# Performance work log

Measured on AMD Instinct MI355X. Metric: run time of the kernel, lower is better.

## Reference

```python
import jax, jax.numpy as jnp
import numpy as np

N_NODES = 50000
N_EDGES = 600000
IN_DIM, HID, OUT_DIM = 128, 128, 64


def setup_inputs() -> dict:
    key = jax.random.key(0)
    ks = jax.random.split(key, 12)
    h = jax.random.normal(ks[0], (N_NODES, IN_DIM), dtype=jnp.float32)
    src = jax.random.randint(ks[1], (N_EDGES,), 0, N_NODES, dtype=jnp.int32)
    dst = jax.random.randint(ks[2], (N_EDGES,), 0, N_NODES, dtype=jnp.int32)
    dims = [(IN_DIM, HID), (HID, HID), (HID, HID), (HID, OUT_DIM)]
    params = {}
    for i, (di, do) in enumerate(dims):
        scale = 1.0 / np.sqrt(di)
        params[f"W{i}"] = jax.random.uniform(ks[3 + i], (di, do), jnp.float32, -scale, scale)
        params[f"b{i}"] = jnp.zeros((do,), jnp.float32)
    return dict(h=h, src=src, dst=dst, **params)


def _gcn_layer(h, W, b, src, dst, norm_src, norm_dst, n_nodes):
    # DGL GraphConv, norm='both': D^{-1/2} A D^{-1/2} (h W) + b
    x = (h * norm_src) @ W              # [N, out]
    agg = jax.ops.segment_sum(x[src], dst, num_segments=n_nodes)
    return agg * norm_dst + b


def reference(h, src, dst, W0, b0, W1, b1, W2, b2, W3, b3):
    n = h.shape[0]
    ones = jnp.ones((src.shape[0],), h.dtype)
    deg_out = jnp.clip(jax.ops.segment_sum(ones, src, num_segments=n), 1.0)
    deg_in = jnp.clip(jax.ops.segment_sum(ones, dst, num_segments=n), 1.0)
    norm_src = (deg_out ** -0.5)[:, None]
    norm_dst = (deg_in ** -0.5)[:, None]
    Ws = [(W0, b0), (W1, b1), (W2, b2), (W3, b3)]
    for i, (W, b) in enumerate(Ws):
        h = _gcn_layer(h, W, b, src, dst, norm_src, norm_dst, n)
        if i != len(Ws) - 1:
            h = jax.nn.relu(h)  # dropout is identity in eval mode
    return h
```

## Files before the change

kernel.cpp:

```cpp
#include <hip/hip_runtime.h>


namespace {

constexpr int NN = 50000;
constexpr int NE = 600000;
constexpr int SCAN_BLK = 256;
constexpr int NBLK = (NN + SCAN_BLK - 1) / SCAN_BLK;
constexpr int EB = (NE + 255) / 256;
constexpr int MFMA0_BLOCKS = (NN / 16 + 3) / 4;
constexpr int WCVT_ELEMS = 16384 * 3 + 8192;
constexpr int WCVT_BLOCKS = WCVT_ELEMS / 256;

typedef unsigned short bhalf;
typedef __attribute__((ext_vector_type(8))) short short8v;
typedef __attribute__((ext_vector_type(4))) float f32x4;

__device__ inline float blo(unsigned int v) {
  return __uint_as_float(v << 16);
}
__device__ inline float bhi(unsigned int v) {
  return __uint_as_float(v & 0xFFFF0000u);
}
__device__ inline unsigned int f2b_bits(float f) {
  unsigned int b = __float_as_uint(f);
  return b + 0x7FFFu + ((b >> 16) & 1u);
}
__device__ inline unsigned int pack2(float lo, float hi) {
  return (f2b_bits(lo) >> 16) | (f2b_bits(hi) & 0xFFFF0000u);
}
__device__ inline bhalf f2b(float f) { return (bhalf)(f2b_bits(f) >> 16); }

__global__ __launch_bounds__(256) void wcvt_kernel(
    const float* __restrict__ W0, const float* __restrict__ W1,
    const float* __restrict__ W2, const float* __restrict__ W3,
    bhalf* __restrict__ wt0, bhalf* __restrict__ wt1,
    bhalf* __restrict__ wt2, bhalf* __restrict__ wt3) {
  int flat = blockIdx.x * 256 + threadIdx.x;
  if (flat < 16384) {
    int j = flat >> 7, k = flat & 127;
    wt0[flat] = f2b(W0[k * 128 + j]);
  } else if (flat < 32768) {
    int f = flat - 16384;
    int j = f >> 7, k = f & 127;
    wt1[f] = f2b(W1[k * 128 + j]);
  } else if (flat < 49152) {
    int f = flat - 32768;
    int j = f >> 7, k = f & 127;
    wt2[f] = f2b(W2[k * 128 + j]);
  } else {
    int f = flat - 49152;
    int j = f >> 7, k = f & 127;
    wt3[f] = f2b(W3[k * 64 + j]);
  }
}

__global__ __launch_bounds__(256, 4) void deg_gemm0_kernel(
    const int* __restrict__ src, const int* __restrict__ dst,
    int* __restrict__ dego, int* __restrict__ degi, int* __restrict__ le,
    const float* __restrict__ h, const bhalf* __restrict__ wt0,
    bhalf* __restrict__ x) {
  if (blockIdx.x < EB) {
    int e = blockIdx.x * 256 + threadIdx.x;
    if (e < NE) {
      atomicAdd(&dego[src[e]], 1);
      le[e] = atomicAdd(&degi[dst[e]], 1);
    }
    return;
  }
  const int lane = threadIdx.x & 63;
  const int wv = threadIdx.x >> 6;
  const int tile = (blockIdx.x - EB) * 4 + wv;
  if (tile >= NN / 16) return;
  const int row0 = tile * 16;
  const size_t arow = (size_t)(row0 + (lane & 15)) * 128;
  const int koff = (lane >> 4) * 8;
  const int bcol = lane & 15;

  f32x4 acc[8];
#pragma unroll
  for (int cf = 0; cf < 8; ++cf) acc[cf] = (f32x4){0.f, 0.f, 0.f, 0.f};

#pragma unroll
  for (int ks = 0; ks < 4; ++ks) {
    const int k0 = ks * 32 + koff;
    float4 ha = *reinterpret_cast<const float4*>(&h[arow + k0]);
    float4 hb = *reinterpret_cast<const float4*>(&h[arow + k0 + 4]);
    short8v av;
    av[0] = (short)f2b(ha.x); av[1] = (short)f2b(ha.y);
    av[2] = (short)f2b(ha.z); av[3] = (short)f2b(ha.w);
    av[4] = (short)f2b(hb.x); av[5] = (short)f2b(hb.y);
    av[6] = (short)f2b(hb.z); av[7] = (short)f2b(hb.w);
#pragma unroll
    for (int cf = 0; cf < 8; ++cf) {
      short8v bv = *reinterpret_cast<const short8v*>(
          &wt0[(size_t)(cf * 16 + bcol) * 128 + k0]);
      acc[cf] = __builtin_amdgcn_mfma_f32_16x16x32_bf16(av, bv, acc[cf], 0, 0, 0);
    }
  }

  const int crow = row0 + ((lane >> 4) << 2);
#pragma unroll
  for (int cf = 0; cf < 8; ++cf) {
#pragma unroll
    for (int r = 0; r < 4; ++r) {
      x[(size_t)(crow + r) * 128 + cf * 16 + bcol] = f2b(acc[cf][r]);
    }
  }
}

__global__ __launch_bounds__(SCAN_BLK) void scan1_norm(const int* __restrict__ dego,
                                                       const int* __restrict__ degi,
                                                       int* __restrict__ bsum,
                                                       float* __restrict__ ns,
                                                       float* __restrict__ nd) {
  __shared__ int ws[SCAN_BLK / 64];
  int i = blockIdx.x * SCAN_BLK + threadIdx.x;
  int v = 0;
  if (i < NN) {
    int din = degi[i];
    int dout = dego[i];
    v = din;
    int a = dout < 1 ? 1 : dout;
    int b = din < 1 ? 1 : din;
    ns[i] = 1.0f / sqrtf((float)a);
    nd[i] = 1.0f / sqrtf((float)b);
  }
#pragma unroll
  for (int off = 32; off; off >>= 1) v += __shfl_down(v, off, 64);
  int lane = threadIdx.x & 63, w = threadIdx.x >> 6;
  if (lane == 0) ws[w] = v;
  __syncthreads();
  if (threadIdx.x == 0) {
    int s = 0;
#pragma unroll
    for (int k = 0; k < SCAN_BLK / 64; ++k) s += ws[k];
    bsum[blockIdx.x] = s;
  }
}

__global__ __launch_bounds__(SCAN_BLK) void scan23(const int* __restrict__ deg,
                                                   const int* __restrict__ bsum,
                                                   int* __restrict__ rowptr) {
  __shared__ int sb[SCAN_BLK];
  __shared__ int s[SCAN_BLK];
  const int t = threadIdx.x;
  int vb = (t < NBLK) ? bsum[t] : 0;
  sb[t] = vb;
  __syncthreads();
  for (int off = 1; off < SCAN_BLK; off <<= 1) {
    int u = (t >= off) ? sb[t - off] : 0;
    __syncthreads();
    sb[t] += u;
    __syncthreads();
  }
  const int pre = (blockIdx.x == 0) ? 0 : sb[blockIdx.x - 1];
  if (blockIdx.x == NBLK - 1 && t == 0) rowptr[NN] = sb[NBLK - 1];

  int i = blockIdx.x * SCAN_BLK + t;
  int v = (i < NN) ? deg[i] : 0;
  s[t] = v;
  __syncthreads();
  for (int off = 1; off < SCAN_BLK; off <<= 1) {
    int u = (t >= off) ? s[t - off] : 0;
    __syncthreads();
    s[t] += u;
    __syncthreads();
  }
  if (i < NN) rowptr[i] = pre + s[t] - v;
}

__global__ void scatter_kernel(const int* __restrict__ src, const int* __restrict__ dst,
                               const int* __restrict__ le, const int* __restrict__ rowptr,
                               int* __restrict__ col) {
  int e = blockIdx.x * blockDim.x + threadIdx.x;
  if (e < NE) col[rowptr[dst[e]] + le[e]] = src[e];
}

template <int DO>
__global__ __launch_bounds__(256, 2) void gemm_mfma(const bhalf* __restrict__ h,
                                                    const bhalf* __restrict__ wt,
                                                    const float* __restrict__ ns,
                                                    bhalf* __restrict__ x) {
  constexpr int CF = DO / 16;
  const int lane = threadIdx.x & 63;
  const int wv = threadIdx.x >> 6;
  const int tile = blockIdx.x * 4 + wv;
  if (tile >= NN / 16) return;
  const int row0 = tile * 16;
  const size_t arow = (size_t)(row0 + (lane & 15)) * 128;
  const int koff = (lane >> 4) * 8;
  const int bcol = lane & 15;

  f32x4 acc[CF];
#pragma unroll
  for (int cf = 0; cf < CF; ++cf) acc[cf] = (f32x4){0.f, 0.f, 0.f, 0.f};

#pragma unroll
  for (int ks = 0; ks < 4; ++ks) {
    const int k0 = ks * 32 + koff;
    short8v av = *reinterpret_cast<const short8v*>(&h[arow + k0]);
#pragma unroll
    for (int cf = 0; cf < CF; ++cf) {
      short8v bv = *reinterpret_cast<const short8v*>(
          &wt[(size_t)(cf * 16 + bcol) * 128 + k0]);
      acc[cf] = __builtin_amdgcn_mfma_f32_16x16x32_bf16(av, bv, acc[cf], 0, 0, 0);
    }
  }

  const int crow = row0 + ((lane >> 4) << 2);
  float nsv[4];
#pragma unroll
  for (int r = 0; r < 4; ++r) nsv[r] = ns[crow + r];
#pragma unroll
  for (int cf = 0; cf < CF; ++cf) {
#pragma unroll
    for (int r = 0; r < 4; ++r) {
      x[(size_t)(crow + r) * DO + cf * 16 + bcol] = f2b(acc[cf][r] * nsv[r]);
    }
  }
}

template <int D, bool RELU, bool NSRC, bool OUTBF>
__global__ __launch_bounds__(256) void gather2_kernel(const bhalf* __restrict__ x,
                                                      const int* __restrict__ rowptr,
                                                      const int* __restrict__ col,
                                                      const float* __restrict__ nd,
                                                      const float* __restrict__ b,
                                                      const float* __restrict__ nsv,
                                                      void* __restrict__ outp) {
  constexpr int LPR = D / 8;
  constexpr int EPW = 64 / LPR;
  const int wid = (blockIdx.x * blockDim.x + threadIdx.x) >> 6;
  const int lane = threadIdx.x & 63;
  const int n0 = wid * 2;
  if (n0 >= NN) return;
  const int n1 = n0 + 1;
  const int sub = lane / LPR;
  const int ci = (lane % LPR) * 8;
  const int beg0 = rowptr[n0], end0 = rowptr[n0 + 1];
  const int beg1 = rowptr[n1], end1 = rowptr[n1 + 1];
  int e0 = beg0 + sub;
  int e1 = beg1 + sub;
  const int d0 = end0 - beg0, d1 = end1 - beg1;
  const int iters = ((d0 > d1 ? d0 : d1) + EPW - 1) / EPW;

  float a0[8], a1[8];
#pragma unroll
  for (int k = 0; k < 8; ++k) { a0[k] = 0.f; a1[k] = 0.f; }

#pragma unroll 2
  for (int it = 0; it < iters; ++it) {
    const bool p0 = e0 < end0;
    const bool p1 = e1 < end1;
    const int ee0 = p0 ? e0 : 0;
    const int ee1 = p1 ? e1 : 0;
    const int c0 = col[ee0];
    const int c1 = col[ee1];
    const float s0 = p0 ? (NSRC ? nsv[c0] : 1.0f) : 0.0f;
    const float s1 = p1 ? (NSRC ? nsv[c1] : 1.0f) : 0.0f;
    const uint4 v0 = *reinterpret_cast<const uint4*>(&x[(size_t)c0 * D + ci]);
    const uint4 v1 = *reinterpret_cast<const uint4*>(&x[(size_t)c1 * D + ci]);
    float f0[8], f1[8];
    f0[0] = blo(v0.x); f0[1] = bhi(v0.x); f0[2] = blo(v0.y); f0[3] = bhi(v0.y);
    f0[4] = blo(v0.z); f0[5] = bhi(v0.z); f0[6] = blo(v0.w); f0[7] = bhi(v0.w);
    f1[0] = blo(v1.x); f1[1] = bhi(v1.x); f1[2] = blo(v1.y); f1[3] = bhi(v1.y);
    f1[4] = blo(v1.z); f1[5] = bhi(v1.z); f1[6] = blo(v1.w); f1[7] = bhi(v1.w);
#pragma unroll
    for (int k = 0; k < 8; ++k) {
      a0[k] = fmaf(s0, f0[k], a0[k]);
      a1[k] = fmaf(s1, f1[k], a1[k]);
    }
    e0 += EPW;
    e1 += EPW;
  }

#pragma unroll
  for (int off = LPR; off < 64; off <<= 1) {
#pragma unroll
    for (int k = 0; k < 8; ++k) {
      a0[k] += __shfl_xor(a0[k], off, 64);
      a1[k] += __shfl_xor(a1[k], off, 64);
    }
  }

  if (lane < 2 * LPR) {
    const bool g0 = lane < LPR;
    const int n = g0 ? n0 : n1;
    const int cw = (g0 ? lane : lane - LPR) * 8;
    const float* acc = g0 ? a0 : a1;
    const float s = nd[n];
    float4 b0 = *reinterpret_cast<const float4*>(&b[cw]);
    float4 b1 = *reinterpret_cast<const float4*>(&b[cw + 4]);
    float r[8];
    r[0] = fmaf(acc[0], s, b0.x); r[1] = fmaf(acc[1], s, b0.y);
    r[2] = fmaf(acc[2], s, b0.z); r[3] = fmaf(acc[3], s, b0.w);
    r[4] = fmaf(acc[4], s, b1.x); r[5] = fmaf(acc[5], s, b1.y);
    r[6] = fmaf(acc[6], s, b1.z); r[7] = fmaf(acc[7], s, b1.w);
    if (RELU) {
#pragma unroll
      for (int k = 0; k < 8; ++k) r[k] = fmaxf(r[k], 0.f);
    }
    if constexpr (OUTBF) {
      bhalf* out = (bhalf*)outp;
      uint4 p;
      p.x = pack2(r[0], r[1]);
      p.y = pack2(r[2], r[3]);
      p.z = pack2(r[4], r[5]);
      p.w = pack2(r[6], r[7]);
      *reinterpret_cast<uint4*>(&out[(size_t)n * D + cw]) = p;
    } else {
      float* out = (float*)outp;
      *reinterpret_cast<float4*>(&out[(size_t)n * D + cw]) =
          make_float4(r[0], r[1], r[2], r[3]);
      *reinterpret_cast<float4*>(&out[(size_t)n * D + cw + 4]) =
          make_float4(r[4], r[5], r[6], r[7]);
    }
  }
}

}

extern "C" void kernel_launch(void* const* d_in, const int* in_sizes, int n_in,
                              void* d_out, int out_size, void* d_ws, size_t ws_size,
                              hipStream_t stream) {
  const float* h0  = (const float*)d_in[0];
  const int*   src = (const int*)d_in[1];
  const int*   dst = (const int*)d_in[2];
  const float* W0 = (const float*)d_in[3];
  const float* b0 = (const float*)d_in[4];
  const float* W1 = (const float*)d_in[5];
  const float* b1 = (const float*)d_in[6];
  const float* W2 = (const float*)d_in[7];
  const float* b2 = (const float*)d_in[8];
  const float* W3 = (const float*)d_in[9];
  const float* b3 = (const float*)d_in[10];
  float* out = (float*)d_out;

  char* w = (char*)d_ws;
  size_t off = 0;
  auto take = [&](size_t bytes) {
    char* p = w + off;
    off = (off + bytes + 255) & ~size_t(255);
    return p;
  };
  int*   deg_out = (int*)take(NN * 4);
  int*   deg_in  = (int*)take(NN * 4);
  float* nsrc    = (float*)take(NN * 4);
  float* ndst    = (float*)take(NN * 4);
  int*   rowptr  = (int*)take((NN + 1) * 4);
  int*   le      = (int*)take(NE * 4);
  int*   col     = (int*)take(NE * 4);
  int*   bsum    = (int*)take(NBLK * 4);
  bhalf* xbuf    = (bhalf*)take((size_t)NN * 128 * 2);
  bhalf* hbuf    = (bhalf*)take((size_t)NN * 128 * 2);
  bhalf* wt0     = (bhalf*)take(128 * 128 * 2);
  bhalf* wt1     = (bhalf*)take(128 * 128 * 2);
  bhalf* wt2     = (bhalf*)take(128 * 128 * 2);
  bhalf* wt3     = (bhalf*)take(64 * 128 * 2);
  (void)ws_size; (void)in_sizes; (void)n_in; (void)out_size;

  hipMemsetAsync(deg_out, 0, (size_t)((char*)nsrc - (char*)deg_out), stream);

  wcvt_kernel<<<WCVT_BLOCKS, 256, 0, stream>>>(W0, W1, W2, W3, wt0, wt1, wt2, wt3);
  deg_gemm0_kernel<<<EB + MFMA0_BLOCKS, 256, 0, stream>>>(
      src, dst, deg_out, deg_in, le, h0, wt0, xbuf);
  scan1_norm<<<NBLK, SCAN_BLK, 0, stream>>>(deg_out, deg_in, bsum, nsrc, ndst);
  scan23<<<NBLK, SCAN_BLK, 0, stream>>>(deg_in, bsum, rowptr);
  scatter_kernel<<<EB, 256, 0, stream>>>(src, dst, le, rowptr, col);

  const int GATHER_BLOCKS = (NN / 2 * 64 + 255) / 256;
  const int MFMA_BLOCKS = (NN / 16 + 3) / 4;

  gather2_kernel<128, true, true, true><<<GATHER_BLOCKS, 256, 0, stream>>>(
      xbuf, rowptr, col, ndst, b0, nsrc, hbuf);
  gemm_mfma<128><<<MFMA_BLOCKS, 256, 0, stream>>>(hbuf, wt1, nsrc, xbuf);
  gather2_kernel<128, true, false, true><<<GATHER_BLOCKS, 256, 0, stream>>>(
      xbuf, rowptr, col, ndst, b1, nullptr, hbuf);
  gemm_mfma<128><<<MFMA_BLOCKS, 256, 0, stream>>>(hbuf, wt2, nsrc, xbuf);
  gather2_kernel<128, true, false, true><<<GATHER_BLOCKS, 256, 0, stream>>>(
      xbuf, rowptr, col, ndst, b2, nullptr, hbuf);
  gemm_mfma<64><<<MFMA_BLOCKS, 256, 0, stream>>>(hbuf, wt3, nsrc, xbuf);
  gather2_kernel<64, false, false, false><<<GATHER_BLOCKS, 256, 0, stream>>>(
      xbuf, rowptr, col, ndst, b3, nullptr, out);
}
```

Baseline: 249.9 us.

## Map several nodes per wave in gather and split degree/GEMM0 kernel

The gather kernel used to assign two nodes per wave, splitting each node's edges across lanes and then reducing with cross-lane shuffles. It now assigns 4 nodes per wave for D=128 and 8 for D=64, with each lane group walking one node's edge list serially and unrolled by 4. This removes the shuffle reduction and keeps more lanes active on output. The trade-off is lane-level imbalance on high-degree nodes and less memory parallelism per node. The fused degree+GEMM0 kernel is also split into a templated fp32-input GEMM followed by a separate degree/atomic kernel, which removes the concurrency the fused launch provided.

```diff
diff --git a/kernel.cpp b/kernel.cpp
--- a/kernel.cpp
+++ b/kernel.cpp
@@ -8,7 +8,7 @@
 constexpr int SCAN_BLK = 256;
 constexpr int NBLK = (NN + SCAN_BLK - 1) / SCAN_BLK;
 constexpr int EB = (NE + 255) / 256;
-constexpr int MFMA0_BLOCKS = (NN / 16 + 3) / 4;
+constexpr int MFMA_BLOCKS = (NN / 16 + 3) / 4;
 constexpr int WCVT_ELEMS = 16384 * 3 + 8192;
 constexpr int WCVT_BLOCKS = WCVT_ELEMS / 256;
 
@@ -55,57 +55,13 @@
   }
 }
 
-__global__ __launch_bounds__(256, 4) void deg_gemm0_kernel(
-    const int* __restrict__ src, const int* __restrict__ dst,
-    int* __restrict__ dego, int* __restrict__ degi, int* __restrict__ le,
-    const float* __restrict__ h, const bhalf* __restrict__ wt0,
-    bhalf* __restrict__ x) {
-  if (blockIdx.x < EB) {
-    int e = blockIdx.x * 256 + threadIdx.x;
-    if (e < NE) {
-      atomicAdd(&dego[src[e]], 1);
-      le[e] = atomicAdd(&degi[dst[e]], 1);
-    }
-    return;
-  }
-  const int lane = threadIdx.x & 63;
-  const int wv = threadIdx.x >> 6;
-  const int tile = (blockIdx.x - EB) * 4 + wv;
-  if (tile >= NN / 16) return;
-  const int row0 = tile * 16;
-  const size_t arow = (size_t)(row0 + (lane & 15)) * 128;
-  const int koff = (lane >> 4) * 8;
-  const int bcol = lane & 15;
-
-  f32x4 acc[8];
-#pragma unroll
-  for (int cf = 0; cf < 8; ++cf) acc[cf] = (f32x4){0.f, 0.f, 0.f, 0.f};
-
-#pragma unroll
-  for (int ks = 0; ks < 4; ++ks) {
-    const int k0 = ks * 32 + koff;
-    float4 ha = *reinterpret_cast<const float4*>(&h[arow + k0]);
-    float4 hb = *reinterpret_cast<const float4*>(&h[arow + k0 + 4]);
-    short8v av;
-    av[0] = (short)f2b(ha.x); av[1] = (short)f2b(ha.y);
-    av[2] = (short)f2b(ha.z); av[3] = (short)f2b(ha.w);
-    av[4] = (short)f2b(hb.x); av[5] = (short)f2b(hb.y);
-    av[6] = (short)f2b(hb.z); av[7] = (short)f2b(hb.w);
-#pragma unroll
-    for (int cf = 0; cf < 8; ++cf) {
-      short8v bv = *reinterpret_cast<const short8v*>(
-          &wt0[(size_t)(cf * 16 + bcol) * 128 + k0]);
-      acc[cf] = __builtin_amdgcn_mfma_f32_16x16x32_bf16(av, bv, acc[cf], 0, 0, 0);
-    }
-  }
-
-  const int crow = row0 + ((lane >> 4) << 2);
-#pragma unroll
-  for (int cf = 0; cf < 8; ++cf) {
-#pragma unroll
-    for (int r = 0; r < 4; ++r) {
-      x[(size_t)(crow + r) * 128 + cf * 16 + bcol] = f2b(acc[cf][r]);
-    }
+__global__ void deg_loc_kernel(const int* __restrict__ src, const int* __restrict__ dst,
+                               int* __restrict__ dego, int* __restrict__ degi,
+                               int* __restrict__ le) {
+  int e = blockIdx.x * blockDim.x + threadIdx.x;
+  if (e < NE) {
+    atomicAdd(&dego[src[e]], 1);
+    le[e] = atomicAdd(&degi[dst[e]], 1);
   }
 }
 
@@ -177,8 +133,8 @@
   if (e < NE) col[rowptr[dst[e]] + le[e]] = src[e];
 }
 
-template <int DO>
-__global__ __launch_bounds__(256, 2) void gemm_mfma(const bhalf* __restrict__ h,
+template <int DO, bool USE_NS, typename TH>
+__global__ __launch_bounds__(256, 2) void gemm_mfma(const TH* __restrict__ h,
                                                     const bhalf* __restrict__ wt,
                                                     const float* __restrict__ ns,
                                                     bhalf* __restrict__ x) {
@@ -199,7 +155,17 @@
 #pragma unroll
   for (int ks = 0; ks < 4; ++ks) {
     const int k0 = ks * 32 + koff;
-    short8v av = *reinterpret_cast<const short8v*>(&h[arow + k0]);
+    short8v av;
+    if constexpr (sizeof(TH) == 4) {
+      float4 ha = *reinterpret_cast<const float4*>(&h[arow + k0]);
+      float4 hb = *reinterpret_cast<const float4*>(&h[arow + k0 + 4]);
+      av[0] = (short)f2b(ha.x); av[1] = (short)f2b(ha.y);
+      av[2] = (short)f2b(ha.z); av[3] = (short)f2b(ha.w);
+      av[4] = (short)f2b(hb.x); av[5] = (short)f2b(hb.y);
+      av[6] = (short)f2b(hb.z); av[7] = (short)f2b(hb.w);
+    } else {
+      av = *reinterpret_cast<const short8v*>(&h[arow + k0]);
+    }
 #pragma unroll
     for (int cf = 0; cf < CF; ++cf) {
       short8v bv = *reinterpret_cast<const short8v*>(
@@ -209,9 +175,11 @@
   }
 
   const int crow = row0 + ((lane >> 4) << 2);
-  float nsv[4];
-#pragma unroll
-  for (int r = 0; r < 4; ++r) nsv[r] = ns[crow + r];
+  float nsv[4] = {1.f, 1.f, 1.f, 1.f};
+  if constexpr (USE_NS) {
+#pragma unroll
+    for (int r = 0; r < 4; ++r) nsv[r] = ns[crow + r];
+  }
 #pragma unroll
   for (int cf = 0; cf < CF; ++cf) {
 #pragma unroll
@@ -222,7 +190,7 @@
 }
 
 template <int D, bool RELU, bool NSRC, bool OUTBF>
-__global__ __launch_bounds__(256) void gather2_kernel(const bhalf* __restrict__ x,
+__global__ __launch_bounds__(256) void gather4_kernel(const bhalf* __restrict__ x,
                                                       const int* __restrict__ rowptr,
                                                       const int* __restrict__ col,
                                                       const float* __restrict__ nd,
@@ -230,92 +198,77 @@
                                                       const float* __restrict__ nsv,
                                                       void* __restrict__ outp) {
   constexpr int LPR = D / 8;
-  constexpr int EPW = 64 / LPR;
+  constexpr int NPW = 64 / LPR;
   const int wid = (blockIdx.x * blockDim.x + threadIdx.x) >> 6;
+  if (wid * NPW >= NN) return;
   const int lane = threadIdx.x & 63;
-  const int n0 = wid * 2;
-  if (n0 >= NN) return;
-  const int n1 = n0 + 1;
-  const int sub = lane / LPR;
+  const int g = lane / LPR;
   const int ci = (lane % LPR) * 8;
-  const int beg0 = rowptr[n0], end0 = rowptr[n0 + 1];
-  const int beg1 = rowptr[n1], end1 = rowptr[n1 + 1];
-  int e0 = beg0 + sub;
-  int e1 = beg1 + sub;
-  const int d0 = end0 - beg0, d1 = end1 - beg1;
-  const int iters = ((d0 > d1 ? d0 : d1) + EPW - 1) / EPW;
-
-  float a0[8], a1[8];
-#pragma unroll
-  for (int k = 0; k < 8; ++k) { a0[k] = 0.f; a1[k] = 0.f; }
-
-#pragma unroll 2
-  for (int it = 0; it < iters; ++it) {
-    const bool p0 = e0 < end0;
-    const bool p1 = e1 < end1;
-    const int ee0 = p0 ? e0 : 0;
-    const int ee1 = p1 ? e1 : 0;
-    const int c0 = col[ee0];
-    const int c1 = col[ee1];
-    const float s0 = p0 ? (NSRC ? nsv[c0] : 1.0f) : 0.0f;
+  const int n = wid * NPW + g;
+  const int beg = rowptr[n];
+  const int end = rowptr[n + 1];
+
+  float a[8];
+#pragma unroll
+  for (int k = 0; k < 8; ++k) a[k] = 0.f;
+
+  for (int e = beg; e < end; e += 4) {
+    const bool p1 = e + 1 < end;
+    const bool p2 = e + 2 < end;
+    const bool p3 = e + 3 < end;
+    const int c0 = col[e];
+    const int c1 = col[p1 ? e + 1 : e];
+    const int c2 = col[p2 ? e + 2 : e];
+    const int c3 = col[p3 ? e + 3 : e];
+    const float s0 = NSRC ? nsv[c0] : 1.0f;
     const float s1 = p1 ? (NSRC ? nsv[c1] : 1.0f) : 0.0f;
+    const float s2 = p2 ? (NSRC ? nsv[c2] : 1.0f) : 0.0f;
+    const float s3 = p3 ? (NSRC ? nsv[c3] : 1.0f) : 0.0f;
     const uint4 v0 = *reinterpret_cast<const uint4*>(&x[(size_t)c0 * D + ci]);
     const uint4 v1 = *reinterpret_cast<const uint4*>(&x[(size_t)c1 * D + ci]);
-    float f0[8], f1[8];
+    const uint4 v2 = *reinterpret_cast<const uint4*>(&x[(size_t)c2 * D + ci]);
+    const uint4 v3 = *reinterpret_cast<const uint4*>(&x[(size_t)c3 * D + ci]);
+    float f0[8], f1[8], f2[8], f3[8];
     f0[0] = blo(v0.x); f0[1] = bhi(v0.x); f0[2] = blo(v0.y); f0[3] = bhi(v0.y);
     f0[4] = blo(v0.z); f0[5] = bhi(v0.z); f0[6] = blo(v0.w); f0[7] = bhi(v0.w);
     f1[0] = blo(v1.x); f1[1] = bhi(v1.x); f1[2] = blo(v1.y); f1[3] = bhi(v1.y);
     f1[4] = blo(v1.z); f1[5] = bhi(v1.z); f1[6] = blo(v1.w); f1[7] = bhi(v1.w);
+    f2[0] = blo(v2.x); f2[1] = bhi(v2.x); f2[2] = blo(v2.y); f2[3] = bhi(v2.y);
+    f2[4] = blo(v2.z); f2[5] = bhi(v2.z); f2[6] = blo(v2.w); f2[7] = bhi(v2.w);
+    f3[0] = blo(v3.x); f3[1] = bhi(v3.x); f3[2] = blo(v3.y); f3[3] = bhi(v3.y);
+    f3[4] = blo(v3.z); f3[5] = bhi(v3.z); f3[6] = blo(v3.w); f3[7] = bhi(v3.w);
 #pragma unroll
     for (int k = 0; k < 8; ++k) {
-      a0[k] = fmaf(s0, f0[k], a0[k]);
-      a1[k] = fmaf(s1, f1[k], a1[k]);
+      a[k] = fmaf(s0, f0[k], fmaf(s1, f1[k], fmaf(s2, f2[k], fmaf(s3, f3[k], a[k]))));
     }
-    e0 += EPW;
-    e1 += EPW;
-  }
-
-#pragma unroll
-  for (int off = LPR; off < 64; off <<= 1) {
-#pragma unroll
-    for (int k = 0; k < 8; ++k) {
-      a0[k] += __shfl_xor(a0[k], off, 64);
-      a1[k] += __shfl_xor(a1[k], off, 64);
-    }
-  }
-
-  if (lane < 2 * LPR) {
-    const bool g0 = lane < LPR;
-    const int n = g0 ? n0 : n1;
-    const int cw = (g0 ? lane : lane - LPR) * 8;
-    const float* acc = g0 ? a0 : a1;
-    const float s = nd[n];
-    float4 b0 = *reinterpret_cast<const float4*>(&b[cw]);
-    float4 b1 = *reinterpret_cast<const float4*>(&b[cw + 4]);
-    float r[8];
-    r[0] = fmaf(acc[0], s, b0.x); r[1] = fmaf(acc[1], s, b0.y);
-    r[2] = fmaf(acc[2], s, b0.z); r[3] = fmaf(acc[3], s, b0.w);
-    r[4] = fmaf(acc[4], s, b1.x); r[5] = fmaf(acc[5], s, b1.y);
-    r[6] = fmaf(acc[6], s, b1.z); r[7] = fmaf(acc[7], s, b1.w);
-    if (RELU) {
-#pragma unroll
-      for (int k = 0; k < 8; ++k) r[k] = fmaxf(r[k], 0.f);
-    }
-    if constexpr (OUTBF) {
-      bhalf* out = (bhalf*)outp;
-      uint4 p;
-      p.x = pack2(r[0], r[1]);
-      p.y = pack2(r[2], r[3]);
-      p.z = pack2(r[4], r[5]);
-      p.w = pack2(r[6], r[7]);
-      *reinterpret_cast<uint4*>(&out[(size_t)n * D + cw]) = p;
-    } else {
-      float* out = (float*)outp;
-      *reinterpret_cast<float4*>(&out[(size_t)n * D + cw]) =
-          make_float4(r[0], r[1], r[2], r[3]);
-      *reinterpret_cast<float4*>(&out[(size_t)n * D + cw + 4]) =
-          make_float4(r[4], r[5], r[6], r[7]);
-    }
+  }
+
+  const float s = nd[n];
+  float4 b0 = *reinterpret_cast<const float4*>(&b[ci]);
+  float4 b1 = *reinterpret_cast<const float4*>(&b[ci + 4]);
+  float r[8];
+  r[0] = fmaf(a[0], s, b0.x); r[1] = fmaf(a[1], s, b0.y);
+  r[2] = fmaf(a[2], s, b0.z); r[3] = fmaf(a[3], s, b0.w);
+  r[4] = fmaf(a[4], s, b1.x); r[5] = fmaf(a[5], s, b1.y);
+  r[6] = fmaf(a[6], s, b1.z); r[7] = fmaf(a[7], s, b1.w);
+  if (RELU) {
+#pragma unroll
+    for (int k = 0; k < 8; ++k) r[k] = fmaxf(r[k], 0.f);
+  }
+  if constexpr (OUTBF) {
+    bhalf* out = (bhalf*)outp;
+    uint4 p;
+    p.x = pack2(r[0], r[1]);
+    p.y = pack2(r[2], r[3]);
+    p.z = pack2(r[4], r[5]);
+    p.w = pack2(r[6], r[7]);
+    *reinterpret_cast<uint4*>(&out[(size_t)n * D + ci]) = p;
+  } else {
+    float* out = (float*)outp;
+    *reinterpret_cast<float4*>(&out[(size_t)n * D + ci]) =
+        make_float4(r[0], r[1], r[2], r[3]);
+    *reinterpret_cast<float4*>(&out[(size_t)n * D + ci + 4]) =
+        make_float4(r[4], r[5], r[6], r[7]);
   }
 }
 
@@ -363,24 +316,24 @@
   hipMemsetAsync(deg_out, 0, (size_t)((char*)nsrc - (char*)deg_out), stream);
 
   wcvt_kernel<<<WCVT_BLOCKS, 256, 0, stream>>>(W0, W1, W2, W3, wt0, wt1, wt2, wt3);
-  deg_gemm0_kernel<<<EB + MFMA0_BLOCKS, 256, 0, stream>>>(
-      src, dst, deg_out, deg_in, le, h0, wt0, xbuf);
+  gemm_mfma<128, false, float><<<MFMA_BLOCKS, 256, 0, stream>>>(h0, wt0, nullptr, xbuf);
+  deg_loc_kernel<<<EB, 256, 0, stream>>>(src, dst, deg_out, deg_in, le);
   scan1_norm<<<NBLK, SCAN_BLK, 0, stream>>>(deg_out, deg_in, bsum, nsrc, ndst);
   scan23<<<NBLK, SCAN_BLK, 0, stream>>>(deg_in, bsum, rowptr);
   scatter_kernel<<<EB, 256, 0, stream>>>(src, dst, le, rowptr, col);
 
-  const int GATHER_BLOCKS = (NN / 2 * 64 + 255) / 256;
-  const int MFMA_BLOCKS = (NN / 16 + 3) / 4;
-
-  gather2_kernel<128, true, true, true><<<GATHER_BLOCKS, 256, 0, stream>>>(
+  const int G4_128 = (NN / 4 * 64) / 256;
+  const int G4_64  = (NN / 8 * 64 + 255) / 256;
+
+  gather4_kernel<128, true, true, true><<<G4_128, 256, 0, stream>>>(
       xbuf, rowptr, col, ndst, b0, nsrc, hbuf);
-  gemm_mfma<128><<<MFMA_BLOCKS, 256, 0, stream>>>(hbuf, wt1, nsrc, xbuf);
-  gather2_kernel<128, true, false, true><<<GATHER_BLOCKS, 256, 0, stream>>>(
+  gemm_mfma<128, true, bhalf><<<MFMA_BLOCKS, 256, 0, stream>>>(hbuf, wt1, nsrc, xbuf);
+  gather4_kernel<128, true, false, true><<<G4_128, 256, 0, stream>>>(
       xbuf, rowptr, col, ndst, b1, nullptr, hbuf);
-  gemm_mfma<128><<<MFMA_BLOCKS, 256, 0, stream>>>(hbuf, wt2, nsrc, xbuf);
-  gather2_kernel<128, true, false, true><<<GATHER_BLOCKS, 256, 0, stream>>>(
+  gemm_mfma<128, true, bhalf><<<MFMA_BLOCKS, 256, 0, stream>>>(hbuf, wt2, nsrc, xbuf);
+  gather4_kernel<128, true, false, true><<<G4_128, 256, 0, stream>>>(
       xbuf, rowptr, col, ndst, b2, nullptr, hbuf);
-  gemm_mfma<64><<<MFMA_BLOCKS, 256, 0, stream>>>(hbuf, wt3, nsrc, xbuf);
-  gather2_kernel<64, false, false, false><<<GATHER_BLOCKS, 256, 0, stream>>>(
+  gemm_mfma<64, true, bhalf><<<MFMA_BLOCKS, 256, 0, stream>>>(hbuf, wt3, nsrc, xbuf);
+  gather4_kernel<64, false, false, false><<<G4_64, 256, 0, stream>>>(
       xbuf, rowptr, col, ndst, b3, nullptr, out);
 }
```

Measured after the change: 250.2 us. Within noise of the previous version (+0.1%).
